# Optimization experiments

Hardware: AMD Instinct MI355X
Metric: run time of the kernel (lower is better)

## Reference

```python
import jax, jax.numpy as jnp
import numpy as np

# init_kwargs baked in as constants (defaults of OHLCVPackedScaler)
OPEN_IDX, HIGH_IDX, LOW_IDX, CLOSE_IDX = 0, 1, 2, 3
VOLUME_IDX, MINUTES_IDX, DOW_IDX = 4, 5, 6
CORRECTION = 1
MIN_SCALE = 1e-5


def _safe_div(numer, denom):
    # uni2ts safe_div: avoid div-by-zero, zero numer where denom==0 yields 0
    return numer / jnp.where(denom == 0, 1.0, denom)


def _group_id(variate_id):
    g = jnp.zeros_like(variate_id)
    ohlc = jnp.isin(variate_id, jnp.array([OPEN_IDX, HIGH_IDX, LOW_IDX, CLOSE_IDX]))
    g = jnp.where(ohlc, 0, g)
    g = jnp.where(variate_id == VOLUME_IDX, 1, g)
    g = jnp.where(variate_id == MINUTES_IDX, 2, g)
    g = jnp.where(variate_id == DOW_IDX, 3, g)
    return g


def setup_inputs() -> dict:
    key = jax.random.key(0)
    k1, k2, k3, k4 = jax.random.split(key, 4)
    B, S, D = 4, 4096, 32
    target = jax.random.normal(k1, (B, S, D), dtype=jnp.float32)
    observed_mask = jax.random.uniform(k2, (B, S, D)) < 0.9
    sample_id = jax.random.randint(k3, (B, S), 0, 8)   # 0 = padding
    variate_id = jax.random.randint(k4, (B, S), 0, 7)  # 0..6 per OHLCV layout
    return {"target": target, "observed_mask": observed_mask,
            "sample_id": sample_id, "variate_id": variate_id}


def reference(target, observed_mask, sample_id, variate_id):
    # original casts to double; we compute stats in fp32 (jax default) and return fp32
    t = target.astype(jnp.float32)
    obs = observed_mask.astype(t.dtype)
    gid = _group_id(variate_id)

    # pairwise (sample_id, group_id) equality mask  [B, S, S]
    id_mask = ((sample_id[..., :, None] == sample_id[..., None, :]) &
               (gid[..., :, None] == gid[..., None, :])).astype(t.dtype)

    # per-token sums over dim, then grouped sums via masked matvec
    tobs = jnp.einsum('bij,bj->bi', id_mask, jnp.sum(obs, axis=-1))[..., None]   # [B,S,1]
    loc = jnp.einsum('bij,bj->bi', id_mask, jnp.sum(t * obs, axis=-1))[..., None]
    loc = _safe_div(loc, tobs)

    var = jnp.einsum('bij,bj->bi', id_mask,
                     jnp.sum((t - loc) ** 2 * obs, axis=-1))[..., None]
    var = _safe_div(var, tobs - CORRECTION)
    scale = jnp.sqrt(var + MIN_SCALE)

    pad = (sample_id == 0)[..., None]
    loc = jnp.where(pad, 0.0, loc).astype(jnp.float32)
    scale = jnp.where(pad, 1.0, scale).astype(jnp.float32)
    return loc, scale
```

## Files before the change

kernel.cpp:

```cpp
#include <hip/hip_runtime.h>
#include <math.h>

#define BB 4
#define SS 4096
#define DD 32
#define NKEY 32
#define NSTAT 3
#define NPART (NKEY * NSTAT)
#define NTOK (BB * SS)
#define TPB 64
#define NBLK (NTOK / TPB)
#define BLK_PER_B (SS / TPB)
#define POISON 0xAAAAAAAAu


__global__ __launch_bounds__(256)
void ohlcv_fused(const float* __restrict__ target,
                 const void* __restrict__ mask,
                 const int* __restrict__ sample_id,
                 const int* __restrict__ variate_id,
                 unsigned* __restrict__ counters,
                 float* __restrict__ partials,
                 float* __restrict__ out) {
    __shared__ float s_acc[NPART];
    __shared__ float s_fin[NPART];
    __shared__ int   s_key[TPB];
    int t = threadIdx.x;
    if (t < NPART) s_acc[t] = 0.0f;

    const unsigned char* mb = (const unsigned char*)mask;
    bool u8 = (__ballot(mb[4 * (t & 63) + 1] != 0) != 0ULL);
    __syncthreads();

    int lt = t >> 5;
    int d  = t & 31;
    int base = blockIdx.x * TPB;

    for (int k = 0; k < TPB / 8; ++k) {
        int slot  = k * 8 + lt;
        int token = base + slot;
        float tg = target[token * DD + d];
        bool obs = u8 ? (mb[token * DD + d] != 0)
                      : (((const int*)mask)[token * DD + d] != 0);
        float o  = obs ? 1.0f    : 0.0f;
        float x  = obs ? tg      : 0.0f;
        float x2 = obs ? tg * tg : 0.0f;
        for (int off = 16; off > 0; off >>= 1) {
            o  += __shfl_down(o,  off, 32);
            x  += __shfl_down(x,  off, 32);
            x2 += __shfl_down(x2, off, 32);
        }
        if (d == 0) {
            int sid = sample_id[token];
            int vid = variate_id[token];
            int g   = (vid <= 3) ? 0 : (vid - 3);
            int key = (sid * 4 + g) * NSTAT;
            s_key[slot] = (sid == 0) ? -1 : key;
            atomicAdd(&s_acc[key + 0], o);
            atomicAdd(&s_acc[key + 1], x);
            atomicAdd(&s_acc[key + 2], x2);
        }
    }
    __syncthreads();

    int b = blockIdx.x / BLK_PER_B;

    if (t < NPART) {
        __hip_atomic_store(&partials[blockIdx.x * NPART + t], s_acc[t],
                           __ATOMIC_RELAXED, __HIP_MEMORY_SCOPE_AGENT);
    }
    __syncthreads();

    if (t == 0) {
        __hip_atomic_fetch_add(&counters[b], 1u,
                               __ATOMIC_RELEASE, __HIP_MEMORY_SCOPE_AGENT);
        while (__hip_atomic_load(&counters[b], __ATOMIC_ACQUIRE,
                                 __HIP_MEMORY_SCOPE_AGENT)
               != POISON + (unsigned)BLK_PER_B) {
            __builtin_amdgcn_s_sleep(2);
        }
    }
    __syncthreads();

    if (t < NPART) {
        const float* p = partials + (size_t)b * BLK_PER_B * NPART + t;
        float s = 0.0f;
        #pragma unroll 8
        for (int q = 0; q < BLK_PER_B; ++q)
            s += __hip_atomic_load(&p[q * NPART], __ATOMIC_RELAXED,
                                   __HIP_MEMORY_SCOPE_AGENT);
        s_fin[t] = s;
    }
    __syncthreads();

    if (t < TPB) {
        int token = base + t;
        int key = s_key[t];
        float loc = 0.0f, scale = 1.0f;
        if (key >= 0) {
            float tobs  = s_fin[key + 0];
            float sum   = s_fin[key + 1];
            float sumsq = s_fin[key + 2];
            float l = sum / (tobs == 0.0f ? 1.0f : tobs);
            float varsum = sumsq - 2.0f * l * sum + l * l * tobs;
            float denom  = tobs - 1.0f;
            float var    = varsum / (denom == 0.0f ? 1.0f : denom);
            loc = l;
            scale = sqrtf(var + 1e-5f);
        }
        out[token] = loc;
        out[NTOK + token] = scale;
    }
}

extern "C" void kernel_launch(void* const* d_in, const int* in_sizes, int n_in,
                              void* d_out, int out_size, void* d_ws, size_t ws_size,
                              hipStream_t stream) {
    const float* target     = (const float*)d_in[0];
    const void*  mask       = d_in[1];
    const int*   sample_id  = (const int*)d_in[2];
    const int*   variate_id = (const int*)d_in[3];
    float*       out        = (float*)d_out;
    unsigned*    counters   = (unsigned*)d_ws;
    float*       partials   = (float*)((char*)d_ws + 16);

    ohlcv_fused<<<NBLK, 256, 0, stream>>>(target, mask, sample_id, variate_id,
                                          counters, partials, out);
}
```

Baseline: 77.48 us.

## Vectorize per-token loads with float4 and reduce over 4-lane groups

```diff
diff --git a/kernel.cpp b/kernel.cpp
--- a/kernel.cpp
+++ b/kernel.cpp
@@ -32,34 +32,54 @@
     bool u8 = (__ballot(mb[4 * (t & 63) + 1] != 0) != 0ULL);
     __syncthreads();
 
-    int lt = t >> 5;
-    int d  = t & 31;
     int base = blockIdx.x * TPB;
 
-    for (int k = 0; k < TPB / 8; ++k) {
-        int slot  = k * 8 + lt;
+    const float4* tg4 = (const float4*)(target + (size_t)base * DD);
+    float4 a0 = tg4[2 * t];
+    float4 a1 = tg4[2 * t + 1];
+    float v[8] = {a0.x, a0.y, a0.z, a0.w, a1.x, a1.y, a1.z, a1.w};
+
+    float ob[8];
+    if (u8) {
+        uint2 mv = ((const uint2*)(mb + (size_t)base * DD))[t];
+        #pragma unroll
+        for (int j = 0; j < 4; ++j) ob[j]     = ((mv.x >> (8 * j)) & 0xFF) ? 1.0f : 0.0f;
+        #pragma unroll
+        for (int j = 0; j < 4; ++j) ob[j + 4] = ((mv.y >> (8 * j)) & 0xFF) ? 1.0f : 0.0f;
+    } else {
+        const int4* mi = (const int4*)((const int*)mask + (size_t)base * DD);
+        int4 b0 = mi[2 * t], b1 = mi[2 * t + 1];
+        ob[0] = b0.x ? 1.0f : 0.0f; ob[1] = b0.y ? 1.0f : 0.0f;
+        ob[2] = b0.z ? 1.0f : 0.0f; ob[3] = b0.w ? 1.0f : 0.0f;
+        ob[4] = b1.x ? 1.0f : 0.0f; ob[5] = b1.y ? 1.0f : 0.0f;
+        ob[6] = b1.z ? 1.0f : 0.0f; ob[7] = b1.w ? 1.0f : 0.0f;
+    }
+
+    float o = 0.0f, x = 0.0f, x2 = 0.0f;
+    #pragma unroll
+    for (int j = 0; j < 8; ++j) {
+        o  += ob[j];
+        x  += ob[j] * v[j];
+        x2 += ob[j] * v[j] * v[j];
+    }
+    #pragma unroll
+    for (int off = 2; off > 0; off >>= 1) {
+        o  += __shfl_down(o,  off, 4);
+        x  += __shfl_down(x,  off, 4);
+        x2 += __shfl_down(x2, off, 4);
+    }
+
+    if ((t & 3) == 0) {
+        int slot  = t >> 2;
         int token = base + slot;
-        float tg = target[token * DD + d];
-        bool obs = u8 ? (mb[token * DD + d] != 0)
-                      : (((const int*)mask)[token * DD + d] != 0);
-        float o  = obs ? 1.0f    : 0.0f;
-        float x  = obs ? tg      : 0.0f;
-        float x2 = obs ? tg * tg : 0.0f;
-        for (int off = 16; off > 0; off >>= 1) {
-            o  += __shfl_down(o,  off, 32);
-            x  += __shfl_down(x,  off, 32);
-            x2 += __shfl_down(x2, off, 32);
-        }
-        if (d == 0) {
-            int sid = sample_id[token];
-            int vid = variate_id[token];
-            int g   = (vid <= 3) ? 0 : (vid - 3);
-            int key = (sid * 4 + g) * NSTAT;
-            s_key[slot] = (sid == 0) ? -1 : key;
-            atomicAdd(&s_acc[key + 0], o);
-            atomicAdd(&s_acc[key + 1], x);
-            atomicAdd(&s_acc[key + 2], x2);
-        }
+        int sid = sample_id[token];
+        int vid = variate_id[token];
+        int g   = (vid <= 3) ? 0 : (vid - 3);
+        int key = (sid * 4 + g) * NSTAT;
+        s_key[slot] = (sid == 0) ? -1 : key;
+        atomicAdd(&s_acc[key + 0], o);
+        atomicAdd(&s_acc[key + 1], x);
+        atomicAdd(&s_acc[key + 2], x2);
     }
     __syncthreads();
 
@@ -67,7 +87,7 @@
 
     if (t < NPART) {
         __hip_atomic_store(&partials[blockIdx.x * NPART + t], s_acc[t],
-                           __ATOMIC_RELAXED, __HIP_MEMORY_SCOPE_AGENT);
+                           __ATOMIC_RELEASE, __HIP_MEMORY_SCOPE_AGENT);
     }
     __syncthreads();
 
@@ -77,18 +97,17 @@
         while (__hip_atomic_load(&counters[b], __ATOMIC_ACQUIRE,
                                  __HIP_MEMORY_SCOPE_AGENT)
                != POISON + (unsigned)BLK_PER_B) {
-            __builtin_amdgcn_s_sleep(2);
+            __builtin_amdgcn_s_sleep(1);
         }
     }
     __syncthreads();
+    __threadfence();
 
     if (t < NPART) {
         const float* p = partials + (size_t)b * BLK_PER_B * NPART + t;
         float s = 0.0f;
         #pragma unroll 8
-        for (int q = 0; q < BLK_PER_B; ++q)
-            s += __hip_atomic_load(&p[q * NPART], __ATOMIC_RELAXED,
-                                   __HIP_MEMORY_SCOPE_AGENT);
+        for (int q = 0; q < BLK_PER_B; ++q) s += p[q * NPART];
         s_fin[t] = s;
     }
     __syncthreads();
@@ -122,7 +141,7 @@
     const int*   variate_id = (const int*)d_in[3];
     float*       out        = (float*)d_out;
     unsigned*    counters   = (unsigned*)d_ws;
-    float*       partials   = (float*)((char*)d_ws + 16);
+    float*       partials   = (float*)((char*)d_ws + 1024);
 
     ohlcv_fused<<<NBLK, 256, 0, stream>>>(target, mask, sample_id, variate_id,
                                           counters, partials, out);
```

Measured after the change: 89.95 us. 1.16x slower.
